# Kernel tuning notes

Hardware: AMD Instinct MI355X
Metric: run time of the kernel (lower is better)

The kernel has to match this reference:

```python
import jax, jax.numpy as jnp
import numpy as np

N = 16384      # nodes
DEG = 20       # avg degree
E = N * DEG    # edges
MUL = 8        # multiplicity of 0e and 1o irreps
NB = 10        # number_of_basis
HID = 64       # fc hidden size
RMAX = 3.5     # max_radius
WNUM = 4 * MUL * MUL  # tp weight numel (4 parity-allowed paths)


def setup_inputs() -> dict:
    key = jax.random.key(0)
    ks = jax.random.split(key, 12)
    f = jax.random.normal(ks[0], (N, 4 * MUL), dtype=jnp.float32)  # 8 scalars + 8 vectors (3 comps)
    pos = jax.random.uniform(ks[1], (N, 3), dtype=jnp.float32) * 2.0  # box keeps dists < RMAX
    rng = np.random.default_rng(0)
    edge_dst = np.repeat(np.arange(N), DEG)
    edge_src = rng.integers(0, N, size=E)
    edge_src = np.where(edge_src == edge_dst, (edge_src + 1) % N, edge_src)
    return {
        'f': f, 'pos': pos,
        'Wq_s': jax.random.normal(ks[2], (MUL, MUL), jnp.float32),
        'Wq_v': jax.random.normal(ks[3], (MUL, MUL), jnp.float32),
        'Wk1': jax.random.normal(ks[4], (NB, HID), jnp.float32),
        'Wk2': jax.random.normal(ks[5], (HID, WNUM), jnp.float32),
        'Wv1': jax.random.normal(ks[6], (NB, HID), jnp.float32),
        'Wv2': jax.random.normal(ks[7], (HID, WNUM), jnp.float32),
        'Wd_s': jax.random.normal(ks[8], (MUL, MUL), jnp.float32),
        'Wd_v': jax.random.normal(ks[9], (MUL, MUL), jnp.float32),
        'edge_src': jnp.asarray(edge_src, jnp.int32),
        'edge_dst': jnp.asarray(edge_dst, jnp.int32),
    }


def _soft_unit_step(x):
    # e3nn soft_unit_step: exp(-1/x) for x>0 else 0; safe for grads
    xs = jnp.where(x > 0, x, 1.0)
    return jnp.where(x > 0, jnp.exp(-1.0 / xs), 0.0)


def _split(x):
    # [*, 4*MUL] -> scalars [*, MUL], vectors [*, MUL, 3]
    return x[:, :MUL], x[:, MUL:].reshape(-1, MUL, 3)


def _fc(x, W1, W2):
    # e3nn FullyConnectedNet: normalized linear -> act -> normalized linear
    h = jax.nn.silu(x @ W1 / jnp.sqrt(jnp.float32(NB)))
    return h @ W2 / jnp.sqrt(jnp.float32(HID))


def _tp(xs, xv, s0, s1, w):
    # fully connected tensor product (in: MULx0e+MULx1o) x (1x0e+1x1o) -> MULx0e+MULx1o
    # w: [E, 4, MUL, MUL]; paths: ss->s, vv->s (dot/sqrt3), sv->v, vs->v
    norm = 1.0 / (MUL ** 0.5 * 2.0 ** 0.5)
    out_s = (jnp.einsum('ei,eio->eo', xs * s0[:, None], w[:, 0]) +
             jnp.einsum('eic,ec,eio->eo', xv, s1, w[:, 1]) / 3.0 ** 0.5) * norm
    out_v = (jnp.einsum('ei,ec,eio->eoc', xs, s1, w[:, 2]) +
             jnp.einsum('eic,eio->eoc', xv * s0[:, None, None], w[:, 3])) * norm
    return out_s, out_v


def reference(f, pos, Wq_s, Wq_v, Wk1, Wk2, Wv1, Wv2, Wd_s, Wd_v, edge_src, edge_dst):
    edge_vec = pos[edge_src] - pos[edge_dst]                      # [E,3]
    r = jnp.linalg.norm(edge_vec, axis=1)                         # [E]
    # soft_one_hot_linspace, basis='smooth_finite', cutoff=True
    values = jnp.linspace(0.0, RMAX, NB + 2)[1:-1]
    step = RMAX / (NB + 1)
    d = (r[:, None] - values) / step
    basis = (1.14136 * np.exp(2.0)) * _soft_unit_step(d + 1.0) * _soft_unit_step(1.0 - d)
    emb = basis * NB ** 0.5                                       # [E,NB]
    cutoff = _soft_unit_step(10.0 * (1.0 - r / RMAX))             # [E]
    # spherical harmonics l=0,1; normalize=True, 'component' norm
    unit = edge_vec / r[:, None]
    s0 = jnp.ones_like(r)
    s1 = (3.0 ** 0.5) * unit                                      # [E,3]
    # query (equivariant linear per irrep)
    fs, fv = _split(f)
    qs = fs @ Wq_s / MUL ** 0.5                                   # [N,MUL]
    qv = jnp.einsum('eic,io->eoc', fv, Wq_v) / MUL ** 0.5         # [N,MUL,3]
    # per-edge tp weights from radial net
    wk = _fc(emb, Wk1, Wk2).reshape(E, 4, MUL, MUL)
    wv = _fc(emb, Wv1, Wv2).reshape(E, 4, MUL, MUL)
    gs, gv = fs[edge_src], fv[edge_src]                           # gather
    ks_, kv_ = _tp(gs, gv, s0, s1, wk)
    vs_, vv_ = _tp(gs, gv, s0, s1, wv)
    # dot tp (q x k -> 0e), shared weights
    qds, qdv = qs[edge_dst], qv[edge_dst]
    logits = (jnp.einsum('ei,ej,ij->e', qds, ks_, Wd_s) +
              jnp.einsum('eic,ejc,ij->e', qdv, kv_, Wd_v) / 3.0 ** 0.5) / (MUL * 2.0 ** 0.5)
    # scatter softmax with cutoff weighting
    mx = jax.ops.segment_max(logits, edge_dst, num_segments=N)
    mx = jnp.where(jnp.isneginf(mx), 0.0, mx)
    expw = cutoff * jnp.exp(logits - mx[edge_dst])
    z = jax.ops.segment_sum(expw, edge_dst, num_segments=N)
    z = jnp.where(z == 0, 1.0, z)
    alpha = expw / z[edge_dst]
    coef = jnp.sqrt(jax.nn.relu(alpha) + 1e-12)                   # [E]
    out_s = jax.ops.segment_sum(coef[:, None] * vs_, edge_dst, num_segments=N)
    out_v = jax.ops.segment_sum(coef[:, None, None] * vv_, edge_dst, num_segments=N)
    return jnp.concatenate([out_s, out_v.reshape(N, 3 * MUL)], axis=1)
```

## Files before the change

### kernel.cpp

```cpp
#include <hip/hip_runtime.h>
#include <hip/hip_bf16.h>
#include <math.h>

#define NN 16384
#define DEG 20
#define EE (NN*DEG)
#define RMAXF 3.5f
#define NGRP 5

typedef __attribute__((ext_vector_type(8))) short short8;
typedef __attribute__((ext_vector_type(4))) float f32x4;

__device__ __forceinline__ float su_f(float x) {
    return x > 0.0f ? __expf(-__builtin_amdgcn_rcpf(x)) : 0.0f;
}
__device__ __forceinline__ ushort f2bf(float x) {
    __hip_bfloat16 h = __float2bfloat16(x);
    return *reinterpret_cast<ushort*>(&h);
}
__device__ __forceinline__ float bf2f(ushort u) {
    return __uint_as_float(((unsigned int)u) << 16);
}

__global__ __launch_bounds__(256, 3) void edge_kernel(
    const float* __restrict__ f,   const float* __restrict__ pos,
    const float* __restrict__ Wqs, const float* __restrict__ Wqv,
    const float* __restrict__ Wds, const float* __restrict__ Wdv,
    const float* __restrict__ Wk1, const float* __restrict__ Wv1,
    const float* __restrict__ Wk2, const float* __restrict__ Wv2,
    const int* __restrict__ esrc,  float* __restrict__ out)
{
    __shared__ float  s_w[2][16][260];
    __shared__ __align__(16) ushort s_hb[2][16][64];
    __shared__ __align__(16) float s_g[2][16][36];
    __shared__ __align__(16) ushort s_embh[2][16][32];
    __shared__ float s_s1[2][16][4];
    __shared__ float s_b[16][9];
    __shared__ __align__(4) ushort s_v[80][34];
    __shared__ float s_lg[80];
    __shared__ float s_cut[80];
    __shared__ float s_mqn[4][32];
    __shared__ int   s_esrc[80];

    const int t = threadIdx.x;
    const int wave = t >> 6, lane = t & 63;
    const int qd = lane >> 4, n = lane & 15;
    const int n0 = blockIdx.x * 4;
    const int E0 = n0 * DEG;

    {
        ushort* z = &s_embh[0][0][0];
        #pragma unroll
        for (int z4 = 0; z4 < 4; z4++) z[t + z4 * 256] = 0;
    }

    if (t < 128) {
        int nd = t >> 5, idx = t & 31;
        const float* fr = f + (size_t)(n0 + nd) * 32;
        const float inv8 = 0.35355339059327373f;
        float o_ = 0.0f;
        if (idx < 8) {
            int j = idx;
            #pragma unroll
            for (int i = 0; i < 8; i++) {
                float qs = 0.0f;
                #pragma unroll
                for (int a = 0; a < 8; a++) qs = fmaf(fr[a], Wqs[a * 8 + i], qs);
                o_ = fmaf(qs * inv8, Wds[i * 8 + j], o_);
            }
        } else {
            int kk = idx - 8;
            int j = kk / 3, c = kk - 3 * j;
            #pragma unroll
            for (int i = 0; i < 8; i++) {
                float qv = 0.0f;
                #pragma unroll
                for (int a = 0; a < 8; a++) qv = fmaf(fr[8 + 3 * a + c], Wqv[a * 8 + i], qv);
                o_ = fmaf(qv * inv8, Wdv[i * 8 + j], o_);
            }
            o_ *= 0.5773502691896258f;
        }
        s_mqn[nd][idx] = o_;
    }
    if (t < 80) s_esrc[t] = esrc[E0 + t];
    __syncthreads();

    short8 b1k, b1v;
    {
        const float invsq10 = 0.31622776601683794f;
        union { ushort u[8]; short8 v; } bk, bv;
        int col = wave * 16 + n;
        #pragma unroll
        for (int j = 0; j < 8; j++) {
            int k0 = qd * 8 + j;
            bk.u[j] = (k0 < 10) ? f2bf(Wk1[k0 * 64 + col] * invsq10) : (ushort)0;
            bv.u[j] = (k0 < 10) ? f2bf(Wv1[k0 * 64 + col] * invsq10) : (ushort)0;
        }
        b1k = bk.v; b1v = bv.v;
    }

    short8 breg[2][2][4];
    #pragma unroll
    for (int net = 0; net < 2; net++) {
        const float* W2 = net ? Wv2 : Wk2;
        #pragma unroll
        for (int s = 0; s < 2; s++)
            #pragma unroll
            for (int jj = 0; jj < 4; jj++) {
                int col = (wave * 4 + jj) * 16 + n;
                union { ushort u[8]; short8 v; } bf;
                #pragma unroll
                for (int j = 0; j < 8; j++) {
                    int k0 = s * 32 + qd * 8 + j;
                    bf.u[j] = f2bf(W2[k0 * 256 + col] * 0.125f);
                }
                breg[net][s][jj] = bf.v;
            }
    }

    {
        int e = t >> 4, rl = t & 15;
        if (rl < 11) {
            int s = s_esrc[e];
            int d = n0;
            float vx = pos[s * 3 + 0] - pos[d * 3 + 0];
            float vy = pos[s * 3 + 1] - pos[d * 3 + 1];
            float vz = pos[s * 3 + 2] - pos[d * 3 + 2];
            float r = sqrtf(vx * vx + vy * vy + vz * vz);
            if (rl < 10) {
                const float step = RMAXF / 11.0f;
                const float invstep = 11.0f / RMAXF;
                const float K = 26.66929988626f;
                float dd = (r - step * (float)(rl + 1)) * invstep;
                s_embh[0][e][rl] = f2bf(K * su_f(dd + 1.0f) * su_f(1.0f - dd));
            } else {
                float invr = __builtin_amdgcn_rcpf(r);
                const float sqrt3 = 1.7320508075688772f;
                s_s1[0][e][0] = sqrt3 * vx * invr;
                s_s1[0][e][1] = sqrt3 * vy * invr;
                s_s1[0][e][2] = sqrt3 * vz * invr;
                s_cut[e] = su_f(10.0f * (1.0f - r / RMAXF));
            }
        }
        if (t < 128) {
            int el = t >> 3, c4 = t & 7;
            int s = s_esrc[el];
            float4 x = *reinterpret_cast<const float4*>(f + (size_t)s * 32 + c4 * 4);
            *reinterpret_cast<float4*>(&s_g[0][el][c4 * 4]) = x;
        }
    }
    __syncthreads();

    for (int g = 0; g < NGRP; g++) {
        const int cb = g & 1, nbuf = cb ^ 1;
        const int le0 = g * 16;
        const bool more = (g + 1 < NGRP);

        float psx = 0.f, psy = 0.f, psz = 0.f, pdx = 0.f, pdy = 0.f, pdz = 0.f;
        float4 pf4 = {0.f, 0.f, 0.f, 0.f};
        {
            int e = t >> 4, rl = t & 15;
            if (more && rl < 11) {
                int s = s_esrc[le0 + 16 + e];
                int d = n0 + (le0 + 16 + e) / DEG;
                psx = pos[s * 3 + 0]; psy = pos[s * 3 + 1]; psz = pos[s * 3 + 2];
                pdx = pos[d * 3 + 0]; pdy = pos[d * 3 + 1]; pdz = pos[d * 3 + 2];
            }
            if (more && t < 128) {
                int el = t >> 3, c4 = t & 7;
                int s = s_esrc[le0 + 16 + el];
                pf4 = *reinterpret_cast<const float4*>(f + (size_t)s * 32 + c4 * 4);
            }
        }

        {
            short8 ea = *(const short8*)&s_embh[cb][n][qd * 8];
            f32x4 dk = {0.0f, 0.0f, 0.0f, 0.0f};
            f32x4 dv = {0.0f, 0.0f, 0.0f, 0.0f};
            dk = __builtin_amdgcn_mfma_f32_16x16x32_bf16(ea, b1k, dk, 0, 0, 0);
            dv = __builtin_amdgcn_mfma_f32_16x16x32_bf16(ea, b1v, dv, 0, 0, 0);
            int hid = wave * 16 + n;
            #pragma unroll
            for (int r = 0; r < 4; r++) {
                int el = qd * 4 + r;
                float ak = dk[r], av = dv[r];
                float hk = ak * __builtin_amdgcn_rcpf(1.0f + __expf(-ak));
                float hv = av * __builtin_amdgcn_rcpf(1.0f + __expf(-av));
                int pos_ = (((hid >> 3) ^ (el & 7)) << 3) | (hid & 7);
                s_hb[0][el][pos_] = f2bf(hk);
                s_hb[1][el][pos_] = f2bf(hv);
            }
            if (t < 128) {
                int el = t >> 3, k = t & 7;
                const float inv_sqrt3 = 0.5773502691896258f;
                s_b[el][k] = (s_g[cb][el][8 + 3 * k + 0] * s_s1[cb][el][0] +
                              s_g[cb][el][8 + 3 * k + 1] * s_s1[cb][el][1] +
                              s_g[cb][el][8 + 3 * k + 2] * s_s1[cb][el][2]) * inv_sqrt3;
            }
        }

        if (more) {
            int e = t >> 4, rl = t & 15;
            if (rl < 11) {
                float vx = psx - pdx, vy = psy - pdy, vz = psz - pdz;
                float r = sqrtf(vx * vx + vy * vy + vz * vz);
                if (rl < 10) {
                    const float step = RMAXF / 11.0f;
                    const float invstep = 11.0f / RMAXF;
                    const float K = 26.66929988626f;
                    float dd = (r - step * (float)(rl + 1)) * invstep;
                    s_embh[nbuf][e][rl] = f2bf(K * su_f(dd + 1.0f) * su_f(1.0f - dd));
                } else {
                    float invr = __builtin_amdgcn_rcpf(r);
                    const float sqrt3 = 1.7320508075688772f;
                    s_s1[nbuf][e][0] = sqrt3 * vx * invr;
                    s_s1[nbuf][e][1] = sqrt3 * vy * invr;
                    s_s1[nbuf][e][2] = sqrt3 * vz * invr;
                    s_cut[le0 + 16 + e] = su_f(10.0f * (1.0f - r / RMAXF));
                }
            }
            if (t < 128) {
                int el = t >> 3, c4 = t & 7;
                *reinterpret_cast<float4*>(&s_g[nbuf][el][c4 * 4]) = pf4;
            }
        }
        __syncthreads();

        #pragma unroll
        for (int net = 0; net < 2; net++) {
            short8 ha0 = *(const short8*)&s_hb[net][n][((qd ^ (n & 7)) << 3)];
            short8 ha1 = *(const short8*)&s_hb[net][n][(((4 + qd) ^ (n & 7)) << 3)];
            #pragma unroll
            for (int jj = 0; jj < 4; jj++) {
                int tt = wave * 4 + jj;
                f32x4 d = {0.0f, 0.0f, 0.0f, 0.0f};
                d = __builtin_amdgcn_mfma_f32_16x16x32_bf16(ha0, breg[net][0][jj], d, 0, 0, 0);
                d = __builtin_amdgcn_mfma_f32_16x16x32_bf16(ha1, breg[net][1][jj], d, 0, 0, 0);
                #pragma unroll
                for (int r = 0; r < 4; r++)
                    s_w[net][4 * qd + r][tt * 16 + n] = d[r];
            }
        }
        __syncthreads();

        {
            int u = t & 127;
            int el = u >> 3, o = u & 7;
            int le = le0 + el;
            float g_[32];
            #pragma unroll
            for (int v4 = 0; v4 < 8; v4++) {
                float4 x = *reinterpret_cast<const float4*>(&s_g[cb][el][v4 * 4]);
                g_[v4 * 4 + 0] = x.x; g_[v4 * 4 + 1] = x.y;
                g_[v4 * 4 + 2] = x.z; g_[v4 * 4 + 3] = x.w;
            }
            const float nrm = 0.25f;

            if (t < 128) {
                int nd = le / DEG;
                const float* wk = s_w[0][el];
                float ks = 0.0f, uk = 0.0f;
                #pragma unroll
                for (int i = 0; i < 8; i++) {
                    ks += g_[i] * wk[i * 8 + o] + s_b[el][i] * wk[64 + i * 8 + o];
                    uk = fmaf(g_[i], wk[128 + i * 8 + o], uk);
                }
                float contrib = s_mqn[nd][o] * (ks * nrm);
                #pragma unroll
                for (int c = 0; c < 3; c++) {
                    float tk = 0.0f;
                    #pragma unroll
                    for (int i = 0; i < 8; i++)
                        tk = fmaf(g_[8 + 3 * i + c], wk[192 + i * 8 + o], tk);
                    float kv_c = nrm * (s_s1[cb][el][c] * uk + tk);
                    contrib = fmaf(s_mqn[nd][8 + 3 * o + c], kv_c, contrib);
                }
                contrib += __shfl_xor(contrib, 1);
                contrib += __shfl_xor(contrib, 2);
                contrib += __shfl_xor(contrib, 4);
                if (o == 0) s_lg[le] = contrib * 0.08838834764831845f;
            } else {
                const float* wv = s_w[1][el];
                float vs = 0.0f, uv = 0.0f;
                #pragma unroll
                for (int i = 0; i < 8; i++) {
                    vs += g_[i] * wv[i * 8 + o] + s_b[el][i] * wv[64 + i * 8 + o];
                    uv = fmaf(g_[i], wv[128 + i * 8 + o], uv);
                }
                s_v[le][o] = f2bf(vs * nrm);
                #pragma unroll
                for (int c = 0; c < 3; c++) {
                    float tv = 0.0f;
                    #pragma unroll
                    for (int i = 0; i < 8; i++)
                        tv = fmaf(g_[8 + 3 * i + c], wv[192 + i * 8 + o], tv);
                    s_v[le][8 + 3 * o + c] = f2bf(nrm * (s_s1[cb][el][c] * uv + tv));
                }
            }
        }
        __syncthreads();
    }

    {
        int base_le = DEG * wave;
        int h32 = lane & 32;
        int hl = lane & 31;
        float lg = -INFINITY, cw = 0.0f;
        if (hl < DEG) {
            lg = s_lg[base_le + hl];
            cw = s_cut[base_le + hl];
        }
        float mx = lg;
        mx = fmaxf(mx, __shfl_xor(mx, 16));
        mx = fmaxf(mx, __shfl_xor(mx, 8));
        mx = fmaxf(mx, __shfl_xor(mx, 4));
        mx = fmaxf(mx, __shfl_xor(mx, 2));
        mx = fmaxf(mx, __shfl_xor(mx, 1));

        float ew = cw * __expf(lg - mx);
        float z = ew;
        z += __shfl_xor(z, 16);
        z += __shfl_xor(z, 8);
        z += __shfl_xor(z, 4);
        z += __shfl_xor(z, 2);
        z += __shfl_xor(z, 1);
        z = (z == 0.0f) ? 1.0f : z;
        float coef = sqrtf(ew * __builtin_amdgcn_rcpf(z) + 1e-12f);

        float acc = 0.0f;
        #pragma unroll
        for (int ee = 0; ee < DEG; ee++) {
            float ce = __shfl(coef, h32 + ee);
            acc = fmaf(ce, bf2f(s_v[base_le + ee][hl]), acc);
        }
        if (lane < 32) out[(size_t)(n0 + wave) * 32 + hl] = acc;
    }
}

extern "C" void kernel_launch(void* const* d_in, const int* in_sizes, int n_in,
                              void* d_out, int out_size, void* d_ws, size_t ws_size,
                              hipStream_t stream) {
    const float* f    = (const float*)d_in[0];
    const float* pos  = (const float*)d_in[1];
    const float* Wqs  = (const float*)d_in[2];
    const float* Wqv  = (const float*)d_in[3];
    const float* Wk1  = (const float*)d_in[4];
    const float* Wk2  = (const float*)d_in[5];
    const float* Wv1  = (const float*)d_in[6];
    const float* Wv2  = (const float*)d_in[7];
    const float* Wds  = (const float*)d_in[8];
    const float* Wdv  = (const float*)d_in[9];
    const int* esrc   = (const int*)d_in[10];
    float* out        = (float*)d_out;

    edge_kernel<<<dim3(NN / 4), dim3(256), 0, stream>>>(
        f, pos, Wqs, Wqv, Wds, Wdv, Wk1, Wv1, Wk2, Wv2, esrc, out);
}
```

Measured before the change: 175.2 us.

## Software-pipeline edge groups to cut one barrier per iteration

Restructures the per-group loop into a deeper software pipeline. The first layer of the radial MLP (hidden activations) for the next group is computed alongside the current group's tensor product. Position and feature gathers are now prefetched two groups ahead, and the second-layer MFMA runs right after the hidden buffer is ready. This removes one __syncthreads per group and overlaps global loads with compute, at the cost of more live registers (dk/dv accumulators and prefetch values kept across phases), which could reduce occupancy.

```diff
diff --git a/kernel.cpp b/kernel.cpp
--- a/kernel.cpp
+++ b/kernel.cpp
@@ -151,54 +151,61 @@
     }
     __syncthreads();
 
+    float psx = 0.f, psy = 0.f, psz = 0.f, pdx = 0.f, pdy = 0.f, pdz = 0.f;
+    float4 pf4 = {0.f, 0.f, 0.f, 0.f};
+    {
+        int e = t >> 4, rl = t & 15;
+        if (rl < 11) {
+            int s = s_esrc[16 + e];
+            int d = n0 + (16 + e) / DEG;
+            psx = pos[s * 3 + 0]; psy = pos[s * 3 + 1]; psz = pos[s * 3 + 2];
+            pdx = pos[d * 3 + 0]; pdy = pos[d * 3 + 1]; pdz = pos[d * 3 + 2];
+        }
+        if (t < 128) {
+            int el = t >> 3, c4 = t & 7;
+            int s = s_esrc[16 + el];
+            pf4 = *reinterpret_cast<const float4*>(f + (size_t)s * 32 + c4 * 4);
+        }
+    }
+    {
+        short8 ea = *(const short8*)&s_embh[0][n][qd * 8];
+        f32x4 dk = {0.0f, 0.0f, 0.0f, 0.0f};
+        f32x4 dv = {0.0f, 0.0f, 0.0f, 0.0f};
+        dk = __builtin_amdgcn_mfma_f32_16x16x32_bf16(ea, b1k, dk, 0, 0, 0);
+        dv = __builtin_amdgcn_mfma_f32_16x16x32_bf16(ea, b1v, dv, 0, 0, 0);
+        int hid = wave * 16 + n;
+        #pragma unroll
+        for (int r = 0; r < 4; r++) {
+            int el = qd * 4 + r;
+            float hk = dk[r] * __builtin_amdgcn_rcpf(1.0f + __expf(-dk[r]));
+            float hv = dv[r] * __builtin_amdgcn_rcpf(1.0f + __expf(-dv[r]));
+            int pos_ = (((hid >> 3) ^ (el & 7)) << 3) | (hid & 7);
+            s_hb[0][el][pos_] = f2bf(hk);
+            s_hb[1][el][pos_] = f2bf(hv);
+        }
+    }
+    __syncthreads();
+
     for (int g = 0; g < NGRP; g++) {
-        const int cb = g & 1, nbuf = cb ^ 1;
+        const int cb = g & 1, nb = cb ^ 1;
         const int le0 = g * 16;
         const bool more = (g + 1 < NGRP);
 
-        float psx = 0.f, psy = 0.f, psz = 0.f, pdx = 0.f, pdy = 0.f, pdz = 0.f;
-        float4 pf4 = {0.f, 0.f, 0.f, 0.f};
-        {
-            int e = t >> 4, rl = t & 15;
-            if (more && rl < 11) {
-                int s = s_esrc[le0 + 16 + e];
-                int d = n0 + (le0 + 16 + e) / DEG;
-                psx = pos[s * 3 + 0]; psy = pos[s * 3 + 1]; psz = pos[s * 3 + 2];
-                pdx = pos[d * 3 + 0]; pdy = pos[d * 3 + 1]; pdz = pos[d * 3 + 2];
-            }
-            if (more && t < 128) {
-                int el = t >> 3, c4 = t & 7;
-                int s = s_esrc[le0 + 16 + el];
-                pf4 = *reinterpret_cast<const float4*>(f + (size_t)s * 32 + c4 * 4);
-            }
-        }
-
-        {
-            short8 ea = *(const short8*)&s_embh[cb][n][qd * 8];
-            f32x4 dk = {0.0f, 0.0f, 0.0f, 0.0f};
-            f32x4 dv = {0.0f, 0.0f, 0.0f, 0.0f};
-            dk = __builtin_amdgcn_mfma_f32_16x16x32_bf16(ea, b1k, dk, 0, 0, 0);
-            dv = __builtin_amdgcn_mfma_f32_16x16x32_bf16(ea, b1v, dv, 0, 0, 0);
-            int hid = wave * 16 + n;
-            #pragma unroll
-            for (int r = 0; r < 4; r++) {
-                int el = qd * 4 + r;
-                float ak = dk[r], av = dv[r];
-                float hk = ak * __builtin_amdgcn_rcpf(1.0f + __expf(-ak));
-                float hv = av * __builtin_amdgcn_rcpf(1.0f + __expf(-av));
-                int pos_ = (((hid >> 3) ^ (el & 7)) << 3) | (hid & 7);
-                s_hb[0][el][pos_] = f2bf(hk);
-                s_hb[1][el][pos_] = f2bf(hv);
-            }
-            if (t < 128) {
-                int el = t >> 3, k = t & 7;
-                const float inv_sqrt3 = 0.5773502691896258f;
-                s_b[el][k] = (s_g[cb][el][8 + 3 * k + 0] * s_s1[cb][el][0] +
-                              s_g[cb][el][8 + 3 * k + 1] * s_s1[cb][el][1] +
-                              s_g[cb][el][8 + 3 * k + 2] * s_s1[cb][el][2]) * inv_sqrt3;
-            }
-        }
-
+        #pragma unroll
+        for (int net = 0; net < 2; net++) {
+            short8 ha0 = *(const short8*)&s_hb[net][n][((qd ^ (n & 7)) << 3)];
+            short8 ha1 = *(const short8*)&s_hb[net][n][(((4 + qd) ^ (n & 7)) << 3)];
+            #pragma unroll
+            for (int jj = 0; jj < 4; jj++) {
+                int tt = wave * 4 + jj;
+                f32x4 d = {0.0f, 0.0f, 0.0f, 0.0f};
+                d = __builtin_amdgcn_mfma_f32_16x16x32_bf16(ha0, breg[net][0][jj], d, 0, 0, 0);
+                d = __builtin_amdgcn_mfma_f32_16x16x32_bf16(ha1, breg[net][1][jj], d, 0, 0, 0);
+                #pragma unroll
+                for (int r = 0; r < 4; r++)
+                    s_w[net][4 * qd + r][tt * 16 + n] = d[r];
+            }
+        }
         if (more) {
             int e = t >> 4, rl = t & 15;
             if (rl < 11) {
@@ -209,40 +216,51 @@
                     const float invstep = 11.0f / RMAXF;
                     const float K = 26.66929988626f;
                     float dd = (r - step * (float)(rl + 1)) * invstep;
-                    s_embh[nbuf][e][rl] = f2bf(K * su_f(dd + 1.0f) * su_f(1.0f - dd));
+                    s_embh[nb][e][rl] = f2bf(K * su_f(dd + 1.0f) * su_f(1.0f - dd));
                 } else {
                     float invr = __builtin_amdgcn_rcpf(r);
                     const float sqrt3 = 1.7320508075688772f;
-                    s_s1[nbuf][e][0] = sqrt3 * vx * invr;
-                    s_s1[nbuf][e][1] = sqrt3 * vy * invr;
-                    s_s1[nbuf][e][2] = sqrt3 * vz * invr;
+                    s_s1[nb][e][0] = sqrt3 * vx * invr;
+                    s_s1[nb][e][1] = sqrt3 * vy * invr;
+                    s_s1[nb][e][2] = sqrt3 * vz * invr;
                     s_cut[le0 + 16 + e] = su_f(10.0f * (1.0f - r / RMAXF));
                 }
             }
             if (t < 128) {
                 int el = t >> 3, c4 = t & 7;
-                *reinterpret_cast<float4*>(&s_g[nbuf][el][c4 * 4]) = pf4;
-            }
+                *reinterpret_cast<float4*>(&s_g[nb][el][c4 * 4]) = pf4;
+            }
+        }
+        if (t < 128) {
+            int el = t >> 3, k = t & 7;
+            const float inv_sqrt3 = 0.5773502691896258f;
+            s_b[el][k] = (s_g[cb][el][8 + 3 * k + 0] * s_s1[cb][el][0] +
+                          s_g[cb][el][8 + 3 * k + 1] * s_s1[cb][el][1] +
+                          s_g[cb][el][8 + 3 * k + 2] * s_s1[cb][el][2]) * inv_sqrt3;
         }
         __syncthreads();
 
-        #pragma unroll
-        for (int net = 0; net < 2; net++) {
-            short8 ha0 = *(const short8*)&s_hb[net][n][((qd ^ (n & 7)) << 3)];
-            short8 ha1 = *(const short8*)&s_hb[net][n][(((4 + qd) ^ (n & 7)) << 3)];
-            #pragma unroll
-            for (int jj = 0; jj < 4; jj++) {
-                int tt = wave * 4 + jj;
-                f32x4 d = {0.0f, 0.0f, 0.0f, 0.0f};
-                d = __builtin_amdgcn_mfma_f32_16x16x32_bf16(ha0, breg[net][0][jj], d, 0, 0, 0);
-                d = __builtin_amdgcn_mfma_f32_16x16x32_bf16(ha1, breg[net][1][jj], d, 0, 0, 0);
-                #pragma unroll
-                for (int r = 0; r < 4; r++)
-                    s_w[net][4 * qd + r][tt * 16 + n] = d[r];
-            }
-        }
-        __syncthreads();
-
+        f32x4 dk = {0.0f, 0.0f, 0.0f, 0.0f};
+        f32x4 dv = {0.0f, 0.0f, 0.0f, 0.0f};
+        if (more) {
+            short8 ea = *(const short8*)&s_embh[nb][n][qd * 8];
+            dk = __builtin_amdgcn_mfma_f32_16x16x32_bf16(ea, b1k, dk, 0, 0, 0);
+            dv = __builtin_amdgcn_mfma_f32_16x16x32_bf16(ea, b1v, dv, 0, 0, 0);
+        }
+        if (g + 2 < NGRP) {
+            int e = t >> 4, rl = t & 15;
+            if (rl < 11) {
+                int s = s_esrc[le0 + 32 + e];
+                int d = n0 + (le0 + 32 + e) / DEG;
+                psx = pos[s * 3 + 0]; psy = pos[s * 3 + 1]; psz = pos[s * 3 + 2];
+                pdx = pos[d * 3 + 0]; pdy = pos[d * 3 + 1]; pdz = pos[d * 3 + 2];
+            }
+            if (t < 128) {
+                int el = t >> 3, c4 = t & 7;
+                int s = s_esrc[le0 + 32 + el];
+                pf4 = *reinterpret_cast<const float4*>(f + (size_t)s * 32 + c4 * 4);
+            }
+        }
         {
             int u = t & 127;
             int el = u >> 3, o = u & 7;
@@ -296,6 +314,18 @@
                         tv = fmaf(g_[8 + 3 * i + c], wv[192 + i * 8 + o], tv);
                     s_v[le][8 + 3 * o + c] = f2bf(nrm * (s_s1[cb][el][c] * uv + tv));
                 }
+            }
+        }
+        if (more) {
+            int hid = wave * 16 + n;
+            #pragma unroll
+            for (int r = 0; r < 4; r++) {
+                int el = qd * 4 + r;
+                float hk = dk[r] * __builtin_amdgcn_rcpf(1.0f + __expf(-dk[r]));
+                float hv = dv[r] * __builtin_amdgcn_rcpf(1.0f + __expf(-dv[r]));
+                int pos_ = (((hid >> 3) ^ (el & 7)) << 3) | (hid & 7);
+                s_hb[0][el][pos_] = f2bf(hk);
+                s_hb[1][el][pos_] = f2bf(hv);
             }
         }
         __syncthreads();
```

Measured after the change: 182.3 us. +4.1%, slower.
